# Kernel tuning notes

Hardware: AMD Instinct MI355X
Metric: run time of the kernel (lower is better)

Reference implementation:

```python
import jax, jax.numpy as jnp
import numpy as np

B, S, T = 1024, 1024, 32  # batch, seq_len, num_tags


def setup_inputs() -> dict:
    key = jax.random.key(0)
    k1, k2, k3, k4 = jax.random.split(key, 4)
    logits = jax.random.normal(k1, (B, S, T), dtype=jnp.float32)
    transitions = jax.random.normal(k2, (T, T), dtype=jnp.float32)
    tags = jax.random.randint(k3, (B, S), 0, T)
    lengths = jax.random.randint(k4, (B,), 1, S + 1)
    return {"logits": logits, "transitions": transitions, "tags": tags, "lengths": lengths}


def _forward_alg(logits, transitions):
    # viterbi_0 = logits[:, 0, :]; then for t>=1:
    # v_next[b, j] = logsumexp_i(v[b, i] + trans[i, j]) + logits[b, t, j]
    v0 = logits[:, 0, :]  # (B, T)
    emits = jnp.swapaxes(logits[:, 1:, :], 0, 1)  # (S-1, B, T)

    def step(v, emit_t):
        v_next = jax.nn.logsumexp(v[:, :, None] + transitions[None, :, :], axis=1) + emit_t
        return v_next, None

    v_final, _ = jax.lax.scan(step, v0, emits)
    return jax.nn.logsumexp(v_final, axis=1)  # (B,)


def _score_sentence(logits, transitions, tags, lengths):
    # emission scores of gold tags, masked to t < length (note: original ignores
    # lengths in the forward algorithm but uses them here, faithfully reproduced)
    emit = jnp.take_along_axis(logits, tags[:, :, None], axis=2)[..., 0]  # (B, S)
    pos = jnp.arange(S)
    emit_mask = (pos[None, :] < lengths[:, None]).astype(logits.dtype)
    score = jnp.sum(emit * emit_mask, axis=1)
    # transition scores trans[tags[t-1], tags[t]] for 1 <= t < length
    trans_sc = transitions[tags[:, :-1], tags[:, 1:]]  # (B, S-1)
    trans_mask = (pos[None, 1:] < lengths[:, None]).astype(logits.dtype)
    score = score + jnp.sum(trans_sc * trans_mask, axis=1)
    return score  # (B,)


def reference(logits, transitions, tags, lengths):
    log_z = _forward_alg(logits, transitions)
    gold = _score_sentence(logits, transitions, tags, lengths)
    return jnp.mean(log_z - gold)
```

## Files before the change

kernel.cpp:

```cpp
#include <hip/hip_runtime.h>

#define NB 1024
#define NS 1024
#define NT 32
#define L2E 1.44269504088896340736f
#define LN2 0.69314718055994530942f

typedef short        bfrag  __attribute__((ext_vector_type(8)));
typedef float        cfrag  __attribute__((ext_vector_type(16)));
typedef __bf16       bf16x2 __attribute__((ext_vector_type(2)));
typedef float        f32x8  __attribute__((ext_vector_type(8)));
typedef float        f32x2  __attribute__((ext_vector_type(2)));
typedef unsigned int u32;
typedef unsigned int u32x2v __attribute__((ext_vector_type(2)));
typedef unsigned int u32x4  __attribute__((ext_vector_type(4)));

__device__ __forceinline__ float fexp2(float x){ return __builtin_amdgcn_exp2f(x); }
__device__ __forceinline__ float flog2(float x){ return __builtin_amdgcn_logf(x); }
__device__ __forceinline__ float frcp (float x){ return __builtin_amdgcn_rcpf(x); }

__device__ __forceinline__ u32 pkbf(float a, float b){
    f32x2 t; t.x = a; t.y = b;
    return __builtin_bit_cast(u32, __builtin_convertvector(t, bf16x2));
}
__device__ __forceinline__ bfrag mk_afrag(f32x8 v){
    u32x4 r;
    r[0] = pkbf(v[0], v[1]); r[1] = pkbf(v[2], v[3]);
    r[2] = pkbf(v[4], v[5]); r[3] = pkbf(v[6], v[7]);
    return __builtin_bit_cast(bfrag, r);
}

#if __has_builtin(__builtin_amdgcn_permlane32_swap)
#define HAVE_PLSWAP 1
#else
#define HAVE_PLSWAP 0
#endif

__device__ __forceinline__ void half_swap(u32 &x, u32 &y, int h){
#if HAVE_PLSWAP
    u32x2v r = __builtin_amdgcn_permlane32_swap(x, y, false, false);
    x = r[0]; y = r[1];
#else
    u32 X  = __shfl_xor(h ? x : y, 32, 64);
    u32 nx = h ? X : x;
    u32 ny = h ? y : X;
    x = nx; y = ny;
#endif
}

__global__ __launch_bounds__(64, 6) void crf_chunk(
    const float* __restrict__ logits, const float* __restrict__ trans,
    const int* __restrict__ tags, const int* __restrict__ lens,
    u32* __restrict__ wmat, float* __restrict__ woff, float* __restrict__ wgold)
{
    __shared__ __align__(16) float dsc[512];

    const int tid = threadIdx.x;
    const int m = tid & 31, h = tid >> 5;
    const int bc = blockIdx.x;
    const int b = bc >> 3, c = bc & 7;

    const float* base = logits + (size_t)b * NS * NT;
    const int*   tgp  = tags + b * NS;
    const int    len  = lens[b];

    f32x8 Et0, Et1;
    #pragma unroll
    for (int j = 0; j < 8; j++){
        Et0[j] = fexp2(L2E * trans[(     8*h + j)*NT + m]);
        Et1[j] = fexp2(L2E * trans[(16 + 8*h + j)*NT + m]);
    }
    const bfrag A0f = mk_afrag(Et0);
    const bfrag A1f = mk_afrag(Et1);

    u32x4 B0v, B1v;
    #pragma unroll
    for (int d = 0; d < 4; d++){
        int k0 = 8*h + 2*d;      u32 v = 0;
        if (k0     == m) v |= 0x3F80u;
        if (k0 + 1 == m) v |= 0x3F800000u;
        B0v[d] = v;
        int k1 = 16 + 8*h + 2*d; v = 0;
        if (k1     == m) v |= 0x3F80u;
        if (k1 + 1 == m) v |= 0x3F800000u;
        B1v[d] = v;
    }

    cfrag zacc;
    #pragma unroll
    for (int q = 0; q < 16; q++) zacc[q] = 0.0f;

    float off = 0.0f;
    float gold = 0.0f;
    if (c == 0){
        float e0 = base[m];
        int  tag0 = tgp[0];
        gold += (h == 0 && m == tag0) ? e0 : 0.0f;
    }

    const int tbeg = c*128 + 1;
    const int L    = (c == 7) ? 127 : 128;

    float eA[4], eB[4]; int gA[4], gB[4];

    auto issue = [&](float (&e)[4], int (&g)[4], int k){
        const int t0 = tbeg + k*8 + 4*h;
        #pragma unroll
        for (int i = 0; i < 4; i++){
            int t = t0 + i; t = t > (NS-1) ? (NS-1) : t;
            e[i] = base[t*NT + m];
            g[i] = tgp[t];
        }
    };
    auto commit = [&](float (&e)[4], int k){
        float* sp = dsc + (k & 1)*256 + (4*h)*32 + m;
        #pragma unroll
        for (int i = 0; i < 4; i++) sp[i*32] = fexp2(L2E * e[i]);
    };

    auto proc = [&](float (&e)[4], int (&g)[4], int k){
        const float* db = dsc + (k & 1)*256 + 4*h;
        const int rem = L - k*8;
        const int nst = rem >= 8 ? 8 : rem;
        #pragma unroll
        for (int i = 0; i < 8; i++){
            if (i < nst){
                const int t = tbeg + k*8 + i;
                cfrag acc = __builtin_amdgcn_mfma_f32_32x32x16_bf16(
                                A0f, __builtin_bit_cast(bfrag, B0v), zacc, 0, 0, 0);
                acc = __builtin_amdgcn_mfma_f32_32x32x16_bf16(
                                A1f, __builtin_bit_cast(bfrag, B1v), acc, 0, 0, 0);

                float4 d0 = *(const float4*)(db + i*32 +  0);
                float4 d1 = *(const float4*)(db + i*32 +  8);
                float4 d2 = *(const float4*)(db + i*32 + 16);
                float4 d3 = *(const float4*)(db + i*32 + 24);
                acc[0]*=d0.x;  acc[1]*=d0.y;  acc[2]*=d0.z;  acc[3]*=d0.w;
                acc[4]*=d1.x;  acc[5]*=d1.y;  acc[6]*=d1.z;  acc[7]*=d1.w;
                acc[8]*=d2.x;  acc[9]*=d2.y;  acc[10]*=d2.z; acc[11]*=d2.w;
                acc[12]*=d3.x; acc[13]*=d3.y; acc[14]*=d3.z; acc[15]*=d3.w;

                const int li = i & 3;
                if (h == (i >> 2) && m == g[li] && t < len) gold += e[li];

                if ((i & 3) == 3){
                    float mx = acc[0];
                    #pragma unroll
                    for (int q = 1; q < 16; q++) mx = fmaxf(mx, acc[q]);
                    mx = fmaxf(mx, __shfl_xor(mx, 32, 64));
                    off += flog2(mx);
                    float s = frcp(mx);
                    #pragma unroll
                    for (int q = 0; q < 16; q++) acc[q] *= s;
                }

                u32 P0 = pkbf(acc[0], acc[1]),  P1 = pkbf(acc[2], acc[3]);
                u32 P2 = pkbf(acc[4], acc[5]),  P3 = pkbf(acc[6], acc[7]);
                u32 P4 = pkbf(acc[8], acc[9]),  P5 = pkbf(acc[10], acc[11]);
                u32 P6 = pkbf(acc[12], acc[13]),P7 = pkbf(acc[14], acc[15]);
                half_swap(P0, P2, h); half_swap(P1, P3, h);
                half_swap(P4, P6, h); half_swap(P5, P7, h);
                B0v[0]=P0; B0v[1]=P1; B0v[2]=P2; B0v[3]=P3;
                B1v[0]=P4; B1v[1]=P5; B1v[2]=P6; B1v[3]=P7;
            }
        }
    };

    issue(eA, gA, 0);
    commit(eA, 0);
    for (int k = 0; k < 16; k += 2){
        issue(eB, gB, k + 1);
        proc(eA, gA, k);
        commit(eB, k + 1);
        if (k + 2 < 16) issue(eA, gA, k + 2);
        proc(eB, gB, k + 1);
        if (k + 2 < 16) commit(eA, k + 2);
    }

    const size_t mb = (size_t)bc * 512;
    #pragma unroll
    for (int d = 0; d < 4; d++){
        wmat[mb + d*64 + tid]     = B0v[d];
        wmat[mb + (4+d)*64 + tid] = B1v[d];
    }
    if (h == 0) woff[bc*32 + m] = off;

    #pragma unroll
    for (int d = 1; d <= 16; d <<= 1) gold += __shfl_xor(gold, d, 64);
    if (tid == 0) wgold[bc] = gold;
}

__global__ __launch_bounds__(64) void crf_combine(
    const float* __restrict__ logits, const float* __restrict__ trans,
    const int* __restrict__ tags, const int* __restrict__ lens,
    const u32* __restrict__ wmat, const float* __restrict__ woff,
    const float* __restrict__ wgold, float* __restrict__ out)
{
    __shared__ __align__(16) float ldsT[NT*NT];
    __shared__ __align__(16) int   ldsTag[NS];
    __shared__ __align__(16) float ldsU[NT];

    const int tid = threadIdx.x;
    const int m   = tid & 31;
    const int b   = blockIdx.x;
    const int len = lens[b];

    #pragma unroll
    for (int i = 0; i < 16; i++) ldsT[tid + i*64] = trans[tid + i*64];
    const int4* tg4 = (const int4*)(tags + b*NS);
    #pragma unroll
    for (int i = 0; i < 4; i++) ((int4*)ldsTag)[tid + i*64] = tg4[tid + i*64];
    __syncthreads();

    float g = 0.0f;
    #pragma unroll
    for (int it = 0; it < 16; it++){
        int t = 1 + tid + it*64;
        if (t < NS && t < len)
            g += ldsT[ldsTag[t-1]*NT + ldsTag[t]];
    }
    if (tid < 8) g += wgold[b*8 + tid];

    float v = fexp2(L2E * logits[(size_t)b*NS*NT + m]);
    float voff = 0.0f;

    const int n  = m;
    const int f  = n >> 4;
    const int hh = (n >> 3) & 1;
    const int di = f*4 + ((n >> 1) & 3);

    for (int cc = 0; cc < 8; cc++){
        const int bcn = b*8 + cc;
        float offm = woff[bcn*32 + m];
        float w = flog2(v) + offm;
        float mw = w;
        #pragma unroll
        for (int d = 1; d <= 16; d <<= 1) mw = fmaxf(mw, __shfl_xor(mw, d, 64));
        float u = fexp2(w - mw);
        if (tid < 32) ldsU[m] = u;
        __syncthreads();

        const uint4*  mp = (const uint4*)(wmat + (size_t)bcn*512 + di*64 + hh*32);
        float acc = 0.0f;
        #pragma unroll
        for (int qq = 0; qq < 8; qq++){
            uint4  md = mp[qq];
            float4 uu = ((const float4*)ldsU)[qq];
            float e0 = __builtin_bit_cast(float, (n&1) ? (md.x & 0xFFFF0000u) : (md.x << 16));
            float e1 = __builtin_bit_cast(float, (n&1) ? (md.y & 0xFFFF0000u) : (md.y << 16));
            float e2 = __builtin_bit_cast(float, (n&1) ? (md.z & 0xFFFF0000u) : (md.z << 16));
            float e3 = __builtin_bit_cast(float, (n&1) ? (md.w & 0xFFFF0000u) : (md.w << 16));
            acc = fmaf(e0, uu.x, acc);
            acc = fmaf(e1, uu.y, acc);
            acc = fmaf(e2, uu.z, acc);
            acc = fmaf(e3, uu.w, acc);
        }
        v = acc;
        voff += mw;
        __syncthreads();
    }

    float s = v;
    #pragma unroll
    for (int d = 1; d <= 16; d <<= 1) s += __shfl_xor(s, d, 64);
    #pragma unroll
    for (int d = 1; d <= 32; d <<= 1) g += __shfl_xor(g, d, 64);
    if (tid == 0){
        float logz = LN2 * (voff + flog2(s));
        atomicAdd(out, (logz - g) * (1.0f / (float)NB));
    }
}

extern "C" void kernel_launch(void* const* d_in, const int* in_sizes, int n_in,
                              void* d_out, int out_size, void* d_ws, size_t ws_size,
                              hipStream_t stream) {
    const float* logits = (const float*)d_in[0];
    const float* trans  = (const float*)d_in[1];
    const int*   tags   = (const int*)d_in[2];
    const int*   lens   = (const int*)d_in[3];

    u32*   wmat  = (u32*)d_ws;
    float* woff  = (float*)(wmat + 8192*512);
    float* wgold = woff + 8192*32;

    hipMemsetAsync(d_out, 0, sizeof(float), stream);
    crf_chunk  <<<8192, 64, 0, stream>>>(logits, trans, tags, lens, wmat, woff, wgold);
    crf_combine<<<1024, 64, 0, stream>>>(logits, trans, tags, lens, wmat, woff, wgold,
                                         (float*)d_out);
}
```

Before: 272.5 us.

## Move gold emission scoring to combine, pack four chunk waves per block, cheaper renormalisation

The gold-path emission gather moves out of the chunk kernel's MFMA recurrence and into the combine kernel, so the hot loop no longer loads tags or checks lengths. The chunk kernel now runs four independent chunk waves per 256-thread block, and its step loop is specialised at compile time for the step count. Renormalisation happens once per 8 steps instead of every 4, and uses a power-of-two scale taken from one element's exponent instead of a full max reduction with log and reciprocal. Scaling is done with packed f32x2 multiplies. Renormalising less often with an exponent-only scale could let values drift further, which risks bf16 overflow or underflow across the 8 steps.

```diff
diff --git a/kernel.cpp b/kernel.cpp
--- a/kernel.cpp
+++ b/kernel.cpp
@@ -17,7 +17,6 @@
 
 __device__ __forceinline__ float fexp2(float x){ return __builtin_amdgcn_exp2f(x); }
 __device__ __forceinline__ float flog2(float x){ return __builtin_amdgcn_logf(x); }
-__device__ __forceinline__ float frcp (float x){ return __builtin_amdgcn_rcpf(x); }
 
 __device__ __forceinline__ u32 pkbf(float a, float b){
     f32x2 t; t.x = a; t.y = b;
@@ -48,21 +47,23 @@
 #endif
 }
 
-__global__ __launch_bounds__(64, 6) void crf_chunk(
+template<int N> struct ic { static constexpr int value = N; };
+union accu { cfrag c; f32x2 p[8]; };
+
+__global__ __launch_bounds__(256, 8) void crf_chunk(
     const float* __restrict__ logits, const float* __restrict__ trans,
-    const int* __restrict__ tags, const int* __restrict__ lens,
-    u32* __restrict__ wmat, float* __restrict__ woff, float* __restrict__ wgold)
+    u32* __restrict__ wmat, float* __restrict__ woff)
 {
-    __shared__ __align__(16) float dsc[512];
+    __shared__ __align__(16) float dscall[4 * 512];
 
     const int tid = threadIdx.x;
-    const int m = tid & 31, h = tid >> 5;
-    const int bc = blockIdx.x;
-    const int b = bc >> 3, c = bc & 7;
+    const int wv  = tid >> 6, lt = tid & 63;
+    const int m   = lt & 31,  h  = lt >> 5;
+    const int bc  = blockIdx.x * 4 + wv;
+    const int b   = bc >> 3,  c  = bc & 7;
+    float* dsc = dscall + wv * 512;
 
     const float* base = logits + (size_t)b * NS * NT;
-    const int*   tgp  = tags + b * NS;
-    const int    len  = lens[b];
 
     f32x8 Et0, Et1;
     #pragma unroll
@@ -91,25 +92,16 @@
     for (int q = 0; q < 16; q++) zacc[q] = 0.0f;
 
     float off = 0.0f;
-    float gold = 0.0f;
-    if (c == 0){
-        float e0 = base[m];
-        int  tag0 = tgp[0];
-        gold += (h == 0 && m == tag0) ? e0 : 0.0f;
-    }
-
     const int tbeg = c*128 + 1;
-    const int L    = (c == 7) ? 127 : 128;
-
-    float eA[4], eB[4]; int gA[4], gB[4];
-
-    auto issue = [&](float (&e)[4], int (&g)[4], int k){
+
+    float eA[4], eB[4];
+
+    auto issue = [&](float (&e)[4], int k){
         const int t0 = tbeg + k*8 + 4*h;
         #pragma unroll
         for (int i = 0; i < 4; i++){
             int t = t0 + i; t = t > (NS-1) ? (NS-1) : t;
             e[i] = base[t*NT + m];
-            g[i] = tgp[t];
         }
     };
     auto commit = [&](float (&e)[4], int k){
@@ -118,83 +110,81 @@
         for (int i = 0; i < 4; i++) sp[i*32] = fexp2(L2E * e[i]);
     };
 
-    auto proc = [&](float (&e)[4], int (&g)[4], int k){
+    auto procN = [&](int k, auto nstc){
+        constexpr int NST = decltype(nstc)::value;
         const float* db = dsc + (k & 1)*256 + 4*h;
-        const int rem = L - k*8;
-        const int nst = rem >= 8 ? 8 : rem;
-        #pragma unroll
-        for (int i = 0; i < 8; i++){
-            if (i < nst){
-                const int t = tbeg + k*8 + i;
-                cfrag acc = __builtin_amdgcn_mfma_f32_32x32x16_bf16(
-                                A0f, __builtin_bit_cast(bfrag, B0v), zacc, 0, 0, 0);
-                acc = __builtin_amdgcn_mfma_f32_32x32x16_bf16(
-                                A1f, __builtin_bit_cast(bfrag, B1v), acc, 0, 0, 0);
-
-                float4 d0 = *(const float4*)(db + i*32 +  0);
-                float4 d1 = *(const float4*)(db + i*32 +  8);
-                float4 d2 = *(const float4*)(db + i*32 + 16);
-                float4 d3 = *(const float4*)(db + i*32 + 24);
-                acc[0]*=d0.x;  acc[1]*=d0.y;  acc[2]*=d0.z;  acc[3]*=d0.w;
-                acc[4]*=d1.x;  acc[5]*=d1.y;  acc[6]*=d1.z;  acc[7]*=d1.w;
-                acc[8]*=d2.x;  acc[9]*=d2.y;  acc[10]*=d2.z; acc[11]*=d2.w;
-                acc[12]*=d3.x; acc[13]*=d3.y; acc[14]*=d3.z; acc[15]*=d3.w;
-
-                const int li = i & 3;
-                if (h == (i >> 2) && m == g[li] && t < len) gold += e[li];
-
-                if ((i & 3) == 3){
-                    float mx = acc[0];
-                    #pragma unroll
-                    for (int q = 1; q < 16; q++) mx = fmaxf(mx, acc[q]);
-                    mx = fmaxf(mx, __shfl_xor(mx, 32, 64));
-                    off += flog2(mx);
-                    float s = frcp(mx);
-                    #pragma unroll
-                    for (int q = 0; q < 16; q++) acc[q] *= s;
-                }
-
-                u32 P0 = pkbf(acc[0], acc[1]),  P1 = pkbf(acc[2], acc[3]);
-                u32 P2 = pkbf(acc[4], acc[5]),  P3 = pkbf(acc[6], acc[7]);
-                u32 P4 = pkbf(acc[8], acc[9]),  P5 = pkbf(acc[10], acc[11]);
-                u32 P6 = pkbf(acc[12], acc[13]),P7 = pkbf(acc[14], acc[15]);
-                half_swap(P0, P2, h); half_swap(P1, P3, h);
-                half_swap(P4, P6, h); half_swap(P5, P7, h);
-                B0v[0]=P0; B0v[1]=P1; B0v[2]=P2; B0v[3]=P3;
-                B1v[0]=P4; B1v[1]=P5; B1v[2]=P6; B1v[3]=P7;
+        #pragma unroll
+        for (int i = 0; i < NST; i++){
+            accu acc;
+            acc.c = __builtin_amdgcn_mfma_f32_32x32x16_bf16(
+                        A0f, __builtin_bit_cast(bfrag, B0v), zacc, 0, 0, 0);
+            acc.c = __builtin_amdgcn_mfma_f32_32x32x16_bf16(
+                        A1f, __builtin_bit_cast(bfrag, B1v), acc.c, 0, 0, 0);
+
+            const f32x2* d0 = (const f32x2*)(db + i*32 +  0);
+            const f32x2* d1 = (const f32x2*)(db + i*32 +  8);
+            const f32x2* d2 = (const f32x2*)(db + i*32 + 16);
+            const f32x2* d3 = (const f32x2*)(db + i*32 + 24);
+            acc.p[0] *= d0[0]; acc.p[1] *= d0[1];
+            acc.p[2] *= d1[0]; acc.p[3] *= d1[1];
+            acc.p[4] *= d2[0]; acc.p[5] *= d2[1];
+            acc.p[6] *= d3[0]; acc.p[7] *= d3[1];
+
+            if (i == 7){
+                float x  = acc.c[0];
+                float xo = __shfl_xor(x, 32, 64);
+                float xs = h ? xo : x;
+                u32 xb = __builtin_bit_cast(u32, xs);
+                int ex = (int)((xb >> 23) & 0xFFu);
+                ex = ex < 24 ? 24 : (ex > 230 ? 230 : ex);
+                off += (float)(ex - 127);
+                f32x2 s2;
+                s2.x = s2.y = __builtin_bit_cast(float, (u32)(254 - ex) << 23);
+                #pragma unroll
+                for (int q = 0; q < 8; q++) acc.p[q] *= s2;
             }
+
+            u32 P0 = pkbf(acc.c[0],  acc.c[1]),  P1 = pkbf(acc.c[2],  acc.c[3]);
+            u32 P2 = pkbf(acc.c[4],  acc.c[5]),  P3 = pkbf(acc.c[6],  acc.c[7]);
+            u32 P4 = pkbf(acc.c[8],  acc.c[9]),  P5 = pkbf(acc.c[10], acc.c[11]);
+            u32 P6 = pkbf(acc.c[12], acc.c[13]), P7 = pkbf(acc.c[14], acc.c[15]);
+            half_swap(P0, P2, h); half_swap(P1, P3, h);
+            half_swap(P4, P6, h); half_swap(P5, P7, h);
+            B0v[0]=P0; B0v[1]=P1; B0v[2]=P2; B0v[3]=P3;
+            B1v[0]=P4; B1v[1]=P5; B1v[2]=P6; B1v[3]=P7;
         }
     };
 
-    issue(eA, gA, 0);
-    commit(eA, 0);
-    for (int k = 0; k < 16; k += 2){
-        issue(eB, gB, k + 1);
-        proc(eA, gA, k);
+    issue(eA, 0); commit(eA, 0);
+    #pragma unroll 1
+    for (int k = 0; k < 14; k += 2){
+        issue(eB, k + 1);
+        procN(k, ic<8>{});
         commit(eB, k + 1);
-        if (k + 2 < 16) issue(eA, gA, k + 2);
-        proc(eB, gB, k + 1);
-        if (k + 2 < 16) commit(eA, k + 2);
-    }
+        issue(eA, k + 2);
+        procN(k + 1, ic<8>{});
+        commit(eA, k + 2);
+    }
+    issue(eB, 15);
+    procN(14, ic<8>{});
+    commit(eB, 15);
+    if (c != 7) procN(15, ic<8>{});
+    else        procN(15, ic<7>{});
 
     const size_t mb = (size_t)bc * 512;
     #pragma unroll
     for (int d = 0; d < 4; d++){
-        wmat[mb + d*64 + tid]     = B0v[d];
-        wmat[mb + (4+d)*64 + tid] = B1v[d];
+        wmat[mb + d*64 + lt]     = B0v[d];
+        wmat[mb + (4+d)*64 + lt] = B1v[d];
     }
     if (h == 0) woff[bc*32 + m] = off;
-
-    #pragma unroll
-    for (int d = 1; d <= 16; d <<= 1) gold += __shfl_xor(gold, d, 64);
-    if (tid == 0) wgold[bc] = gold;
 }
 
 __global__ __launch_bounds__(64) void crf_combine(
     const float* __restrict__ logits, const float* __restrict__ trans,
     const int* __restrict__ tags, const int* __restrict__ lens,
     const u32* __restrict__ wmat, const float* __restrict__ woff,
-    const float* __restrict__ wgold, float* __restrict__ out)
+    float* __restrict__ out)
 {
     __shared__ __align__(16) float ldsT[NT*NT];
     __shared__ __align__(16) int   ldsTag[NS];
@@ -204,6 +194,7 @@
     const int m   = tid & 31;
     const int b   = blockIdx.x;
     const int len = lens[b];
+    const float* lgb = logits + (size_t)b * NS * NT;
 
     #pragma unroll
     for (int i = 0; i < 16; i++) ldsT[tid + i*64] = trans[tid + i*64];
@@ -215,13 +206,15 @@
     float g = 0.0f;
     #pragma unroll
     for (int it = 0; it < 16; it++){
-        int t = 1 + tid + it*64;
-        if (t < NS && t < len)
-            g += ldsT[ldsTag[t-1]*NT + ldsTag[t]];
-    }
-    if (tid < 8) g += wgold[b*8 + tid];
-
-    float v = fexp2(L2E * logits[(size_t)b*NS*NT + m]);
+        int t = tid + it*64;
+        if (t < len){
+            int tg = ldsTag[t];
+            g += lgb[t*NT + tg];
+            if (t >= 1) g += ldsT[ldsTag[t-1]*NT + tg];
+        }
+    }
+
+    float v = fexp2(L2E * lgb[m]);
     float voff = 0.0f;
 
     const int n  = m;
@@ -240,7 +233,7 @@
         if (tid < 32) ldsU[m] = u;
         __syncthreads();
 
-        const uint4*  mp = (const uint4*)(wmat + (size_t)bcn*512 + di*64 + hh*32);
+        const uint4* mp = (const uint4*)(wmat + (size_t)bcn*512 + di*64 + hh*32);
         float acc = 0.0f;
         #pragma unroll
         for (int qq = 0; qq < 8; qq++){
@@ -279,12 +272,11 @@
     const int*   tags   = (const int*)d_in[2];
     const int*   lens   = (const int*)d_in[3];
 
-    u32*   wmat  = (u32*)d_ws;
-    float* woff  = (float*)(wmat + 8192*512);
-    float* wgold = woff + 8192*32;
+    u32*   wmat = (u32*)d_ws;
+    float* woff = (float*)(wmat + 8192*512);
 
     hipMemsetAsync(d_out, 0, sizeof(float), stream);
-    crf_chunk  <<<8192, 64, 0, stream>>>(logits, trans, tags, lens, wmat, woff, wgold);
-    crf_combine<<<1024, 64, 0, stream>>>(logits, trans, tags, lens, wmat, woff, wgold,
+    crf_chunk  <<<2048, 256, 0, stream>>>(logits, trans, wmat, woff);
+    crf_combine<<<1024, 64, 0, stream>>>(logits, trans, tags, lens, wmat, woff,
                                          (float*)d_out);
 }
```

After: 266.9 us. 2.1% less time.
